# Kernel tuning notes

Hardware: AMD Instinct MI355X
Metric: run time of the kernel (lower is better)

The kernel has to match this reference:

```python
import jax, jax.numpy as jnp
import numpy as np

D_IN, D_OUT, H, L = 18, 2, 128, 2  # from load_pretrained config; bidirectional


def _uniform(key, shape, scale):
    return jax.random.uniform(key, shape, jnp.float32, -scale, scale)


def setup_inputs() -> dict:
    key = jax.random.key(0)
    ks = jax.random.split(key, 32)
    B, T = 64, 2048
    s = 1.0 / np.sqrt(H)
    inp = {"x": jax.random.normal(ks[0], (B, T, D_IN), jnp.float32)}
    i = 1
    for l in range(L):
        d_in_l = D_IN if l == 0 else 2 * H
        for suf in ("", "r"):
            inp[f"w_ih_l{l}{suf}"] = _uniform(ks[i], (3 * H, d_in_l), s); i += 1
            inp[f"w_hh_l{l}{suf}"] = _uniform(ks[i], (3 * H, H), s); i += 1
            inp[f"b_ih_l{l}{suf}"] = _uniform(ks[i], (3 * H,), s); i += 1
            inp[f"b_hh_l{l}{suf}"] = _uniform(ks[i], (3 * H,), s); i += 1
    inp["fc_w"] = _uniform(ks[i], (D_OUT, 2 * H), 1.0 / np.sqrt(2 * H)); i += 1
    inp["fc_b"] = _uniform(ks[i], (D_OUT,), 1.0 / np.sqrt(2 * H))
    return inp


def gru_dir(x, w_ih, w_hh, b_ih, b_hh, reverse):
    # x: [B,T,Din] -> [B,T,H], PyTorch GRU gate math (r,z,n ordering)
    B, T, _ = x.shape
    xg = jnp.einsum('btd,gd->btg', x, w_ih) + b_ih  # [B,T,3H], batched GEMM once
    if reverse:
        xg = xg[:, ::-1]
    def step(h, xt):
        gh = h @ w_hh.T + b_hh
        xr, xz, xn = jnp.split(xt, 3, axis=-1)
        hr, hz, hn = jnp.split(gh, 3, axis=-1)
        r = jax.nn.sigmoid(xr + hr)
        z = jax.nn.sigmoid(xz + hz)
        n = jnp.tanh(xn + r * hn)
        h_new = (1.0 - z) * n + z * h
        return h_new, h_new
    h0 = jnp.zeros((B, H), x.dtype)
    _, ys = jax.lax.scan(step, h0, jnp.swapaxes(xg, 0, 1))  # scan over time
    ys = jnp.swapaxes(ys, 0, 1)
    if reverse:
        ys = ys[:, ::-1]
    return ys


def gru_forward(x, params):
    h = x
    for l in range(L):
        fwd = gru_dir(h, params[f"w_ih_l{l}"], params[f"w_hh_l{l}"],
                      params[f"b_ih_l{l}"], params[f"b_hh_l{l}"], False)
        bwd = gru_dir(h, params[f"w_ih_l{l}r"], params[f"w_hh_l{l}r"],
                      params[f"b_ih_l{l}r"], params[f"b_hh_l{l}r"], True)
        h = jnp.concatenate([fwd, bwd], axis=-1)  # [B,T,2H]; dropout off (eval)
    return h


def reference(x, w_ih_l0, w_hh_l0, b_ih_l0, b_hh_l0,
              w_ih_l0r, w_hh_l0r, b_ih_l0r, b_hh_l0r,
              w_ih_l1, w_hh_l1, b_ih_l1, b_hh_l1,
              w_ih_l1r, w_hh_l1r, b_ih_l1r, b_hh_l1r,
              fc_w, fc_b):
    params = dict(w_ih_l0=w_ih_l0, w_hh_l0=w_hh_l0, b_ih_l0=b_ih_l0, b_hh_l0=b_hh_l0,
                  w_ih_l0r=w_ih_l0r, w_hh_l0r=w_hh_l0r, b_ih_l0r=b_ih_l0r, b_hh_l0r=b_hh_l0r,
                  w_ih_l1=w_ih_l1, w_hh_l1=w_hh_l1, b_ih_l1=b_ih_l1, b_hh_l1=b_hh_l1,
                  w_ih_l1r=w_ih_l1r, w_hh_l1r=w_hh_l1r, b_ih_l1r=b_ih_l1r, b_hh_l1r=b_hh_l1r)
    h = gru_forward(x, params)
    return jnp.einsum('bth,oh->bto', h, fc_w) + fc_b  # [B,T,D_OUT]
```

## Files before the change

### kernel.cpp

```cpp
#include <hip/hip_runtime.h>
#include <hip/hip_bf16.h>

#define B_   64
#define T_   2048
#define H_   128
#define G_   384
#define D0_  18
#define WIN  4
#define RING 8
#define NW   (T_ / WIN)

typedef __hip_bfloat16 bf16;
typedef __attribute__((ext_vector_type(4))) float f32x4;
typedef __attribute__((ext_vector_type(8))) short s16x8;

#define LOG2E  1.4426950408889634f
#define NEGL2E (-1.4426950408889634f)
#define TWOL2E (2.8853900817779268f)

__device__ __forceinline__ short f2bs(float v) {
    bf16 b = __float2bfloat16(v);
    return *reinterpret_cast<short*>(&b);
}
__device__ __forceinline__ unsigned short f2bu(float v) {
    bf16 b = __float2bfloat16(v);
    return *reinterpret_cast<unsigned short*>(&b);
}
__device__ __forceinline__ uint2 pk_bf16x4(float a, float b, float c, float d) {
    uint2 r;
    asm("v_cvt_pk_bf16_f32 %0, %1, %2" : "=v"(r.x) : "v"(a), "v"(b));
    asm("v_cvt_pk_bf16_f32 %0, %1, %2" : "=v"(r.y) : "v"(c), "v"(d));
    return r;
}
#define MFMA16(A, B, C) __builtin_amdgcn_mfma_f32_16x16x32_bf16((A), (B), (C), 0, 0, 0)

__device__ __forceinline__ void step_sync() {
    __asm__ volatile("s_waitcnt lgkmcnt(0)" ::: "memory");
    __builtin_amdgcn_s_barrier();
    __asm__ volatile("" ::: "memory");
}

__device__ __forceinline__ float gru_update(float yr, float yz, float aN,
                                            float aX, float h) {
    const float Er = __builtin_amdgcn_exp2f(yr);
    const float rg = __builtin_amdgcn_rcpf(1.0f + Er);
    const float En = __builtin_amdgcn_exp2f(fmaf(rg, aN, aX));
    const float Ez = __builtin_amdgcn_exp2f(yz);
    const float p  = fmaf(En, Ez, -Ez);
    const float q2 = fmaf(h, En, h);
    const float t1 = Ez + 1.0f;
    const float dn = fmaf(En, t1, t1);
    return (p + q2) * __builtin_amdgcn_rcpf(dn);
}


__global__ __launch_bounds__(512) void gru_l0_mfma(
    const float* __restrict__ x,
    const float* __restrict__ wih_f, const float* __restrict__ whh_f,
    const float* __restrict__ bih_f, const float* __restrict__ bhh_f,
    const float* __restrict__ wih_r, const float* __restrict__ whh_r,
    const float* __restrict__ bih_r, const float* __restrict__ bhh_r,
    bf16* __restrict__ l0h)
{
    __shared__ __align__(16) bf16 hring[RING][2048];
    __shared__ __align__(16) bf16 xbuf[2][WIN][512];

    const int bx   = blockIdx.x;
    const int dir  = bx >> 2;
    const int bg   = bx & 3;
    const int b0   = bg * 16;
    const int tid  = threadIdx.x;
    const int lane = tid & 63;
    const int wv   = tid >> 6;
    const int col  = lane & 15;
    const int quad = lane >> 4;

    const float* Wih = dir ? wih_r : wih_f;
    const float* Whh = dir ? whh_r : whh_f;
    const float* Bih = dir ? bih_r : bih_f;
    const float* Bhh = dir ? bhh_r : bhh_f;

    const float GSC[3] = {NEGL2E, NEGL2E, TWOL2E};

    s16x8 wfr[3][4], wxf[3];
    #pragma unroll
    for (int g = 0; g < 3; ++g) {
        const float sc = GSC[g];
        const float* wrow = Whh + (size_t)(g * H_ + wv * 16 + col) * H_;
        #pragma unroll
        for (int kt = 0; kt < 4; ++kt) {
            const float* p = wrow + kt * 32 + quad * 8;
            s16x8 f;
            #pragma unroll
            for (int i = 0; i < 8; ++i) f[i] = f2bs(p[i] * sc);
            wfr[g][kt] = f;
        }
        const float* xrow = Wih + (size_t)(g * H_ + wv * 16 + col) * D0_;
        s16x8 fx;
        #pragma unroll
        for (int i = 0; i < 8; ++i) {
            const int k = quad * 8 + i;
            fx[i] = (k < D0_) ? f2bs(xrow[k] * sc) : (short)0;
        }
        wxf[g] = fx;
    }
    f32x4 sR, sZ, sX, sN;
    #pragma unroll
    for (int r = 0; r < 4; ++r) {
        const int j = wv * 16 + quad * 4 + r;
        sR[r] = (Bih[j]        + Bhh[j])      * NEGL2E;
        sZ[r] = (Bih[H_ + j]   + Bhh[H_ + j]) * NEGL2E;
        sX[r] = Bih[2*H_ + j]  * TWOL2E;
        sN[r] = Bhh[2*H_ + j]  * TWOL2E;
    }

    const int wkt   = wv >> 1;
    const int wl    = (((wv << 1) + (quad >> 1)) & 3) * 16 + col;
    const int woff  = wkt * 512 + wl * 8 + (quad & 1) * 4;

    for (int i = tid; i < 2048; i += 512) hring[0][i] = __float2bfloat16(0.0f);
    #pragma unroll
    for (int k = 0; k < 4; ++k) {
        const int i = tid + k * 512;
        const int si = i >> 9, rem = i & 511;
        const int m = (rem >> 5) & 15, c = rem & 31;
        const int t = dir ? (T_ - 1 - si) : si;
        const float v = (c < D0_) ? x[((size_t)(b0 + m) * T_ + t) * D0_ + c] : 0.0f;
        xbuf[0][si][((c >> 3) * 16 + m) * 8 + (c & 7)] = __float2bfloat16(v);
    }
    __syncthreads();

    float hprev[4] = {0.f, 0.f, 0.f, 0.f};
    float xv[4];

    for (int w = 0; w < NW; ++w) {
        const int par = w & 1;
        s16x8 axf[WIN];
        #pragma unroll
        for (int si = 0; si < WIN; ++si)
            axf[si] = *(const s16x8*)&xbuf[par][si][lane * 8];

        #pragma unroll
        for (int si = 0; si < WIN; ++si) {
            const int s  = w * WIN + si;
            const int rb = s & (RING - 1);
            const int wb = (s + 1) & (RING - 1);

            s16x8 hfr[4];
            #pragma unroll
            for (int kt = 0; kt < 4; ++kt)
                hfr[kt] = *(const s16x8*)&hring[rb][kt * 512 + lane * 8];

            f32x4 aR = MFMA16(wxf[0], axf[si], sR);
            f32x4 aZ = MFMA16(wxf[1], axf[si], sZ);
            f32x4 aX = MFMA16(wxf[2], axf[si], sX);
            f32x4 aN = sN;
            #pragma unroll
            for (int kt = 0; kt < 4; ++kt) {
                aR = MFMA16(wfr[0][kt], hfr[kt], aR);
                aZ = MFMA16(wfr[1][kt], hfr[kt], aZ);
                aN = MFMA16(wfr[2][kt], hfr[kt], aN);
            }

            if (si == 1 && w > 0) {
                #pragma unroll
                for (int k = 0; k < 2; ++k) {
                    const int c  = tid + k * 512;
                    const int dt = c >> 8, m = (c >> 4) & 15, jo = c & 15;
                    const int fs = (w - 1) * WIN + dt;
                    const int t  = dir ? (T_ - 1 - fs) : fs;
                    const uint4 v = *(const uint4*)
                        &hring[(fs + 1) & (RING - 1)][(jo >> 2) * 512 + ((jo & 3) * 16 + m) * 8];
                    *(uint4*)(l0h + ((size_t)(b0 + m) * T_ + t) * 256 + dir * H_ + jo * 8) = v;
                }
            }

            if (si == 0 && w + 1 < NW) {
                #pragma unroll
                for (int k = 0; k < 4; ++k) {
                    const int i = tid + k * 512;
                    const int sj = i >> 9, rem = i & 511;
                    const int m = (rem >> 5) & 15, c = rem & 31;
                    const int s2 = (w + 1) * WIN + sj;
                    const int t2 = dir ? (T_ - 1 - s2) : s2;
                    xv[k] = (c < D0_) ? x[((size_t)(b0 + m) * T_ + t2) * D0_ + c] : 0.0f;
                }
            }

            float hn4[4];
            #pragma unroll
            for (int r = 0; r < 4; ++r) {
                const float hn = gru_update(aR[r], aZ[r], aN[r], aX[r], hprev[r]);
                hprev[r] = hn;
                hn4[r] = hn;
            }
            *(uint2*)&hring[wb][woff] = pk_bf16x4(hn4[0], hn4[1], hn4[2], hn4[3]);

            if (si == 3 && w + 1 < NW) {
                #pragma unroll
                for (int k = 0; k < 4; ++k) {
                    const int i = tid + k * 512;
                    const int sj = i >> 9, rem = i & 511;
                    const int m = (rem >> 5) & 15, c = rem & 31;
                    xbuf[par ^ 1][sj][((c >> 3) * 16 + m) * 8 + (c & 7)] =
                        __float2bfloat16(xv[k]);
                }
            }
            step_sync();
        }
    }
    #pragma unroll
    for (int k = 0; k < 2; ++k) {
        const int c  = tid + k * 512;
        const int dt = c >> 8, m = (c >> 4) & 15, jo = c & 15;
        const int fs = (NW - 1) * WIN + dt;
        const int t  = dir ? (T_ - 1 - fs) : fs;
        const uint4 v = *(const uint4*)
            &hring[(fs + 1) & (RING - 1)][(jo >> 2) * 512 + ((jo & 3) * 16 + m) * 8];
        *(uint4*)(l0h + ((size_t)(b0 + m) * T_ + t) * 256 + dir * H_ + jo * 8) = v;
    }
}

__global__ __launch_bounds__(256, 2) void xg_gemm_mfma(
    const bf16* __restrict__ A,
    const float* __restrict__ w_f, const float* __restrict__ w_r,
    const float* __restrict__ bi_f, const float* __restrict__ bi_r,
    const float* __restrict__ bh_f, const float* __restrict__ bh_r,
    bf16* __restrict__ xg_f, bf16* __restrict__ xg_r)
{
    __shared__ short As[128 * 40];
    __shared__ short Ws[128 * 40];
    __shared__ float Bias_s[128];

    const int dir  = blockIdx.z;
    const float* W   = dir ? w_r : w_f;
    const float* bi  = dir ? bi_r : bi_f;
    const float* bh  = dir ? bh_r : bh_f;
    bf16* xg         = dir ? xg_r : xg_f;

    const int tid  = threadIdx.x;
    const int lane = tid & 63;
    const int wv   = tid >> 6;
    const int col  = lane & 15;
    const int quad = lane >> 4;
    const int bx   = blockIdx.x;
    const int bg   = bx >> 8;
    const int t0   = (bx & 255) * 8;
    const int g    = blockIdx.y;
    const int m0   = g * 128;

    const float sc = (g < 2) ? NEGL2E : TWOL2E;
    const f32x4 z4 = {0.f, 0.f, 0.f, 0.f};

    if (tid < 128) {
        const int n = m0 + tid;
        Bias_s[tid] = (bi[n] + ((n < 2 * H_) ? bh[n] : 0.0f)) * sc;
    }

    f32x4 acc[2][8];
    #pragma unroll
    for (int mt = 0; mt < 2; ++mt)
        #pragma unroll
        for (int nt = 0; nt < 8; ++nt) acc[mt][nt] = z4;

    for (int k0 = 0; k0 < 256; k0 += 32) {
        #pragma unroll
        for (int i = 0; i < 2; ++i) {
            const int c = tid + i * 256;
            const int row = c >> 2, q4 = c & 3;
            const int dt = row >> 4, m = row & 15;
            *(uint4*)&As[row * 40 + q4 * 8] =
                *(const uint4*)(A + (((size_t)(bg * 16 + m) * T_ + t0 + dt) * 256)
                                + k0 + q4 * 8);
        }
        #pragma unroll
        for (int i = 0; i < 4; ++i) {
            const int c = tid + i * 256;
            const int row = c >> 3, q = c & 7;
            const float4 v = *(const float4*)(W + (size_t)(m0 + row) * 256 + k0 + q * 4);
            ushort4 u;
            u.x = f2bu(v.x * sc); u.y = f2bu(v.y * sc);
            u.z = f2bu(v.z * sc); u.w = f2bu(v.w * sc);
            *(ushort4*)&Ws[row * 40 + q * 4] = u;
        }
        __syncthreads();

        s16x8 wfr[2], hfr[8];
        #pragma unroll
        for (int mt = 0; mt < 2; ++mt)
            wfr[mt] = *(const s16x8*)&Ws[(wv * 32 + mt * 16 + col) * 40 + quad * 8];
        #pragma unroll
        for (int nt = 0; nt < 8; ++nt)
            hfr[nt] = *(const s16x8*)&As[(nt * 16 + col) * 40 + quad * 8];

        #pragma unroll
        for (int mt = 0; mt < 2; ++mt)
            #pragma unroll
            for (int nt = 0; nt < 8; ++nt)
                acc[mt][nt] = MFMA16(wfr[mt], hfr[nt], acc[mt][nt]);
        __syncthreads();
    }

    #pragma unroll
    for (int mt = 0; mt < 2; ++mt) {
        const int jt = wv * 2 + mt;
        float bv[4];
        #pragma unroll
        for (int r = 0; r < 4; ++r)
            bv[r] = Bias_s[wv * 32 + mt * 16 + quad * 4 + r];
        #pragma unroll
        for (int nt = 0; nt < 8; ++nt) {
            const uint2 o = pk_bf16x4(acc[mt][nt][0] + bv[0],
                                      acc[mt][nt][1] + bv[1],
                                      acc[mt][nt][2] + bv[2],
                                      acc[mt][nt][3] + bv[3]);
            const size_t idx = ((((size_t)bg * T_ + t0 + nt) * 3 + g) * 8 + jt) * 64
                             + quad * 16 + col;
            ((uint2*)xg)[idx] = o;
        }
    }
}

__global__ __launch_bounds__(512) void gru_l1_mfma(
    const bf16* __restrict__ xg_f, const bf16* __restrict__ xg_r,
    const float* __restrict__ whh_f, const float* __restrict__ bhh_f,
    const float* __restrict__ whh_r, const float* __restrict__ bhh_r,
    bf16* __restrict__ l1h, int fixed_dir)
{
    __shared__ __align__(16) bf16 hring[RING][2048];

    const int bx   = blockIdx.x;
    const int dir  = (fixed_dir >= 0) ? fixed_dir : (bx >> 2);
    const int bg   = bx & 3;
    const int b0   = bg * 16;
    const int tid  = threadIdx.x;
    const int lane = tid & 63;
    const int wv   = tid >> 6;
    const int col  = lane & 15;
    const int quad = lane >> 4;

    const bf16*  XG  = dir ? xg_r : xg_f;
    const float* Whh = dir ? whh_r : whh_f;
    const float* Bhh = dir ? bhh_r : bhh_f;

    const float GSC[3] = {NEGL2E, NEGL2E, TWOL2E};

    s16x8 wfr[3][4];
    #pragma unroll
    for (int g = 0; g < 3; ++g) {
        const float sc = GSC[g];
        const float* wrow = Whh + (size_t)(g * H_ + wv * 16 + col) * H_;
        #pragma unroll
        for (int kt = 0; kt < 4; ++kt) {
            const float* p = wrow + kt * 32 + quad * 8;
            s16x8 f;
            #pragma unroll
            for (int i = 0; i < 8; ++i) f[i] = f2bs(p[i] * sc);
            wfr[g][kt] = f;
        }
    }
    f32x4 sN;
    #pragma unroll
    for (int r = 0; r < 4; ++r)
        sN[r] = Bhh[2*H_ + wv * 16 + quad * 4 + r] * TWOL2E;

    const int wkt  = wv >> 1;
    const int wl   = (((wv << 1) + (quad >> 1)) & 3) * 16 + col;
    const int woff = wkt * 512 + wl * 8 + (quad & 1) * 4;

    for (int i = tid; i < 2048; i += 512) hring[0][i] = __float2bfloat16(0.0f);

    const uint2* xgb = (const uint2*)XG + ((size_t)bg * T_) * 3 * 8 * 64;
    const int lidx = wv * 64 + lane;

    uint2 xcur[WIN][3], xnxt[WIN][3];
    #pragma unroll
    for (int si = 0; si < WIN; ++si) {
        const int t = dir ? (T_ - 1 - si) : si;
        #pragma unroll
        for (int g = 0; g < 3; ++g)
            xcur[si][g] = xgb[((size_t)t * 3 + g) * 512 + lidx];
    }
    __syncthreads();

    float hprev[4] = {0.f, 0.f, 0.f, 0.f};

    for (int w = 0; w < NW; ++w) {
        #pragma unroll
        for (int si = 0; si < WIN; ++si) {
            const int s  = w * WIN + si;
            const int rb = s & (RING - 1);
            const int wb = (s + 1) & (RING - 1);

            s16x8 hfr[4];
            #pragma unroll
            for (int kt = 0; kt < 4; ++kt)
                hfr[kt] = *(const s16x8*)&hring[rb][kt * 512 + lane * 8];

            const uint2 xr2 = xcur[si][0], xz2 = xcur[si][1], xn2 = xcur[si][2];
            const f32x4 seedR = (f32x4){
                __uint_as_float(xr2.x << 16), __uint_as_float(xr2.x & 0xffff0000u),
                __uint_as_float(xr2.y << 16), __uint_as_float(xr2.y & 0xffff0000u)};
            const f32x4 seedZ = (f32x4){
                __uint_as_float(xz2.x << 16), __uint_as_float(xz2.x & 0xffff0000u),
                __uint_as_float(xz2.y << 16), __uint_as_float(xz2.y & 0xffff0000u)};
            const float xnf[4] = {
                __uint_as_float(xn2.x << 16), __uint_as_float(xn2.x & 0xffff0000u),
                __uint_as_float(xn2.y << 16), __uint_as_float(xn2.y & 0xffff0000u)};

            f32x4 aR = seedR, aZ = seedZ, aN = sN;
            #pragma unroll
            for (int kt = 0; kt < 4; ++kt) {
                aR = MFMA16(wfr[0][kt], hfr[kt], aR);
                aZ = MFMA16(wfr[1][kt], hfr[kt], aZ);
                aN = MFMA16(wfr[2][kt], hfr[kt], aN);
            }

            if (si == 1 && w > 0) {
                #pragma unroll
                for (int k = 0; k < 2; ++k) {
                    const int c  = tid + k * 512;
                    const int dt = c >> 8, m = (c >> 4) & 15, jo = c & 15;
                    const int fs = (w - 1) * WIN + dt;
                    const int t  = dir ? (T_ - 1 - fs) : fs;
                    const uint4 v = *(const uint4*)
                        &hring[(fs + 1) & (RING - 1)][(jo >> 2) * 512 + ((jo & 3) * 16 + m) * 8];
                    *(uint4*)(l1h + ((size_t)(b0 + m) * T_ + t) * 256 + dir * H_ + jo * 8) = v;
                }
            }

            if (si == 0 && w + 1 < NW) {
                #pragma unroll
                for (int sj = 0; sj < WIN; ++sj) {
                    const int s2 = (w + 1) * WIN + sj;
                    const int t2 = dir ? (T_ - 1 - s2) : s2;
                    #pragma unroll
                    for (int g = 0; g < 3; ++g)
                        xnxt[sj][g] = xgb[((size_t)t2 * 3 + g) * 512 + lidx];
                }
            }

            float hn4[4];
            #pragma unroll
            for (int r = 0; r < 4; ++r) {
                const float hn = gru_update(aR[r], aZ[r], aN[r], xnf[r], hprev[r]);
                hprev[r] = hn;
                hn4[r] = hn;
            }
            *(uint2*)&hring[wb][woff] = pk_bf16x4(hn4[0], hn4[1], hn4[2], hn4[3]);

            step_sync();
        }

        #pragma unroll
        for (int si = 0; si < WIN; ++si) {
            xcur[si][0] = xnxt[si][0];
            xcur[si][1] = xnxt[si][1];
            xcur[si][2] = xnxt[si][2];
        }
    }
    #pragma unroll
    for (int k = 0; k < 2; ++k) {
        const int c  = tid + k * 512;
        const int dt = c >> 8, m = (c >> 4) & 15, jo = c & 15;
        const int fs = (NW - 1) * WIN + dt;
        const int t  = dir ? (T_ - 1 - fs) : fs;
        const uint4 v = *(const uint4*)
            &hring[(fs + 1) & (RING - 1)][(jo >> 2) * 512 + ((jo & 3) * 16 + m) * 8];
        *(uint4*)(l1h + ((size_t)(b0 + m) * T_ + t) * 256 + dir * H_ + jo * 8) = v;
    }
}

__global__ __launch_bounds__(256, 2) void fc_kernel(
    const bf16* __restrict__ h, const float* __restrict__ fcw,
    const float* __restrict__ fcb, float* __restrict__ out)
{
    __shared__ float w0[256], w1[256];
    const int tid = threadIdx.x;
    w0[tid] = fcw[tid];
    w1[tid] = fcw[256 + tid];
    __syncthreads();

    const size_t bt = (size_t)blockIdx.x * 256 + tid;
    const bf16* hp = h + bt * 256;
    float s0 = fcb[0], s1 = fcb[1];
    #pragma unroll 4
    for (int k8 = 0; k8 < 32; ++k8) {
        const uint4 u = *(const uint4*)(hp + k8 * 8);
        const unsigned uu[4] = {u.x, u.y, u.z, u.w};
        #pragma unroll
        for (int p = 0; p < 4; ++p) {
            const float v0 = __uint_as_float(uu[p] << 16);
            const float v1 = __uint_as_float(uu[p] & 0xffff0000u);
            const int k = k8 * 8 + p * 2;
            s0 = fmaf(w0[k], v0, s0);     s1 = fmaf(w1[k], v0, s1);
            s0 = fmaf(w0[k + 1], v1, s0); s1 = fmaf(w1[k + 1], v1, s1);
        }
    }
    out[bt * 2]     = s0;
    out[bt * 2 + 1] = s1;
}

extern "C" void kernel_launch(void* const* d_in, const int* in_sizes, int n_in,
                              void* d_out, int out_size, void* d_ws, size_t ws_size,
                              hipStream_t stream)
{
    if (n_in < 19) return;
    const float* x     = (const float*)d_in[0];
    const float* wih0  = (const float*)d_in[1];
    const float* whh0  = (const float*)d_in[2];
    const float* bih0  = (const float*)d_in[3];
    const float* bhh0  = (const float*)d_in[4];
    const float* wih0r = (const float*)d_in[5];
    const float* whh0r = (const float*)d_in[6];
    const float* bih0r = (const float*)d_in[7];
    const float* bhh0r = (const float*)d_in[8];
    const float* wih1  = (const float*)d_in[9];
    const float* whh1  = (const float*)d_in[10];
    const float* bih1  = (const float*)d_in[11];
    const float* bhh1  = (const float*)d_in[12];
    const float* wih1r = (const float*)d_in[13];
    const float* whh1r = (const float*)d_in[14];
    const float* bih1r = (const float*)d_in[15];
    const float* bhh1r = (const float*)d_in[16];
    const float* fcw   = (const float*)d_in[17];
    const float* fcb   = (const float*)d_in[18];
    float* out = (float*)d_out;

    const size_t nBT  = (size_t)B_ * T_;
    const size_t hh_b = nBT * 2 * H_ * sizeof(bf16);
    const size_t xg_b = nBT * G_ * sizeof(bf16);
    const size_t xg_el = nBT * G_;

    if (ws_size >= hh_b + 2 * xg_b) {
        bf16* l0h = (bf16*)d_ws;
        bf16* xgf = (bf16*)((char*)d_ws + hh_b);
        bf16* xgr = xgf + xg_el;

        gru_l0_mfma<<<dim3(8), dim3(512), 0, stream>>>(
            x, wih0, whh0, bih0, bhh0, wih0r, whh0r, bih0r, bhh0r, l0h);
        xg_gemm_mfma<<<dim3(1024, 3, 2), dim3(256), 0, stream>>>(
            l0h, wih1, wih1r, bih1, bih1r, bhh1, bhh1r, xgf, xgr);
        gru_l1_mfma<<<dim3(8), dim3(512), 0, stream>>>(
            xgf, xgr, whh1, bhh1, whh1r, bhh1r, l0h, -1);
        fc_kernel<<<dim3((int)(nBT / 256)), dim3(256), 0, stream>>>(l0h, fcw, fcb, out);
    } else if (ws_size >= 2 * hh_b + xg_b) {
        bf16* l0h = (bf16*)d_ws;
        bf16* xg  = (bf16*)((char*)d_ws + hh_b);
        bf16* l1h = (bf16*)((char*)d_ws + hh_b + xg_b);

        gru_l0_mfma<<<dim3(8), dim3(512), 0, stream>>>(
            x, wih0, whh0, bih0, bhh0, wih0r, whh0r, bih0r, bhh0r, l0h);
        xg_gemm_mfma<<<dim3(1024, 3, 1), dim3(256), 0, stream>>>(
            l0h, wih1, wih1, bih1, bih1, bhh1, bhh1, xg, xg);
        gru_l1_mfma<<<dim3(4), dim3(512), 0, stream>>>(
            xg, xg, whh1, bhh1, whh1r, bhh1r, l1h, 0);
        xg_gemm_mfma<<<dim3(1024, 3, 1), dim3(256), 0, stream>>>(
            l0h, wih1r, wih1r, bih1r, bih1r, bhh1r, bhh1r, xg, xg);
        gru_l1_mfma<<<dim3(4), dim3(512), 0, stream>>>(
            xg, xg, whh1, bhh1, whh1r, bhh1r, l1h, 1);
        fc_kernel<<<dim3((int)(nBT / 256)), dim3(256), 0, stream>>>(l1h, fcw, fcb, out);
    }
}
```

Baseline: 2.509 ms.

## Duplicate recurrent MFMA across two wave halves to split gate updates

Both recurrent GRU kernels now run 1024 threads per block instead of 512. The upper eight waves redundantly compute the same MFMA tiles as the lower eight, and each half applies the gate nonlinearity to only two of the four accumulator rows, writing packed bf16 pairs. The aim is to halve the serial transcendental and update work on the per-step critical path and to spread the output and prefetch stores over more threads. The cost is doubled MFMA issue, more register pressure under the 1024-thread bound, and a wider barrier every step.

```diff
diff --git a/kernel.cpp b/kernel.cpp
--- a/kernel.cpp
+++ b/kernel.cpp
@@ -25,6 +25,11 @@
 __device__ __forceinline__ unsigned short f2bu(float v) {
     bf16 b = __float2bfloat16(v);
     return *reinterpret_cast<unsigned short*>(&b);
+}
+__device__ __forceinline__ unsigned pk_bf16x2(float a, float b) {
+    unsigned r;
+    asm("v_cvt_pk_bf16_f32 %0, %1, %2" : "=v"(r) : "v"(a), "v"(b));
+    return r;
 }
 __device__ __forceinline__ uint2 pk_bf16x4(float a, float b, float c, float d) {
     uint2 r;
@@ -54,7 +59,7 @@
 }
 
 
-__global__ __launch_bounds__(512) void gru_l0_mfma(
+__global__ __launch_bounds__(1024) void gru_l0_mfma(
     const float* __restrict__ x,
     const float* __restrict__ wih_f, const float* __restrict__ whh_f,
     const float* __restrict__ bih_f, const float* __restrict__ bhh_f,
@@ -71,7 +76,8 @@
     const int b0   = bg * 16;
     const int tid  = threadIdx.x;
     const int lane = tid & 63;
-    const int wv   = tid >> 6;
+    const int wv   = (tid >> 6) & 7;
+    const int half = tid >> 9;
     const int col  = lane & 15;
     const int quad = lane >> 4;
 
@@ -116,12 +122,12 @@
 
     const int wkt   = wv >> 1;
     const int wl    = (((wv << 1) + (quad >> 1)) & 3) * 16 + col;
-    const int woff  = wkt * 512 + wl * 8 + (quad & 1) * 4;
-
-    for (int i = tid; i < 2048; i += 512) hring[0][i] = __float2bfloat16(0.0f);
-    #pragma unroll
-    for (int k = 0; k < 4; ++k) {
-        const int i = tid + k * 512;
+    const int woff  = wkt * 512 + wl * 8 + (quad & 1) * 4 + half * 2;
+
+    for (int i = tid; i < 2048; i += 1024) hring[0][i] = __float2bfloat16(0.0f);
+    #pragma unroll
+    for (int k = 0; k < 2; ++k) {
+        const int i = tid + k * 1024;
         const int si = i >> 9, rem = i & 511;
         const int m = (rem >> 5) & 15, c = rem & 31;
         const int t = dir ? (T_ - 1 - si) : si;
@@ -130,8 +136,8 @@
     }
     __syncthreads();
 
-    float hprev[4] = {0.f, 0.f, 0.f, 0.f};
-    float xv[4];
+    float hprev[2] = {0.f, 0.f};
+    float xv[2];
 
     for (int w = 0; w < NW; ++w) {
         const int par = w & 1;
@@ -163,22 +169,19 @@
             }
 
             if (si == 1 && w > 0) {
+                const int c  = tid;
+                const int dt = c >> 8, m = (c >> 4) & 15, jo = c & 15;
+                const int fs = (w - 1) * WIN + dt;
+                const int t  = dir ? (T_ - 1 - fs) : fs;
+                const uint4 v = *(const uint4*)
+                    &hring[(fs + 1) & (RING - 1)][(jo >> 2) * 512 + ((jo & 3) * 16 + m) * 8];
+                *(uint4*)(l0h + ((size_t)(b0 + m) * T_ + t) * 256 + dir * H_ + jo * 8) = v;
+            }
+
+            if (si == 0 && w + 1 < NW) {
                 #pragma unroll
                 for (int k = 0; k < 2; ++k) {
-                    const int c  = tid + k * 512;
-                    const int dt = c >> 8, m = (c >> 4) & 15, jo = c & 15;
-                    const int fs = (w - 1) * WIN + dt;
-                    const int t  = dir ? (T_ - 1 - fs) : fs;
-                    const uint4 v = *(const uint4*)
-                        &hring[(fs + 1) & (RING - 1)][(jo >> 2) * 512 + ((jo & 3) * 16 + m) * 8];
-                    *(uint4*)(l0h + ((size_t)(b0 + m) * T_ + t) * 256 + dir * H_ + jo * 8) = v;
-                }
-            }
-
-            if (si == 0 && w + 1 < NW) {
-                #pragma unroll
-                for (int k = 0; k < 4; ++k) {
-                    const int i = tid + k * 512;
+                    const int i = tid + k * 1024;
                     const int sj = i >> 9, rem = i & 511;
                     const int m = (rem >> 5) & 15, c = rem & 31;
                     const int s2 = (w + 1) * WIN + sj;
@@ -187,19 +190,19 @@
                 }
             }
 
-            float hn4[4];
-            #pragma unroll
-            for (int r = 0; r < 4; ++r) {
-                const float hn = gru_update(aR[r], aZ[r], aN[r], aX[r], hprev[r]);
-                hprev[r] = hn;
-                hn4[r] = hn;
-            }
-            *(uint2*)&hring[wb][woff] = pk_bf16x4(hn4[0], hn4[1], hn4[2], hn4[3]);
+            const float yr0 = half ? aR[2] : aR[0], yr1 = half ? aR[3] : aR[1];
+            const float yz0 = half ? aZ[2] : aZ[0], yz1 = half ? aZ[3] : aZ[1];
+            const float an0 = half ? aN[2] : aN[0], an1 = half ? aN[3] : aN[1];
+            const float ax0 = half ? aX[2] : aX[0], ax1 = half ? aX[3] : aX[1];
+            const float hn0 = gru_update(yr0, yz0, an0, ax0, hprev[0]);
+            const float hn1 = gru_update(yr1, yz1, an1, ax1, hprev[1]);
+            hprev[0] = hn0; hprev[1] = hn1;
+            *(unsigned*)&hring[wb][woff] = pk_bf16x2(hn0, hn1);
 
             if (si == 3 && w + 1 < NW) {
                 #pragma unroll
-                for (int k = 0; k < 4; ++k) {
-                    const int i = tid + k * 512;
+                for (int k = 0; k < 2; ++k) {
+                    const int i = tid + k * 1024;
                     const int sj = i >> 9, rem = i & 511;
                     const int m = (rem >> 5) & 15, c = rem & 31;
                     xbuf[par ^ 1][sj][((c >> 3) * 16 + m) * 8 + (c & 7)] =
@@ -209,9 +212,8 @@
             step_sync();
         }
     }
-    #pragma unroll
-    for (int k = 0; k < 2; ++k) {
-        const int c  = tid + k * 512;
+    {
+        const int c  = tid;
         const int dt = c >> 8, m = (c >> 4) & 15, jo = c & 15;
         const int fs = (NW - 1) * WIN + dt;
         const int t  = dir ? (T_ - 1 - fs) : fs;
@@ -321,7 +323,7 @@
     }
 }
 
-__global__ __launch_bounds__(512) void gru_l1_mfma(
+__global__ __launch_bounds__(1024) void gru_l1_mfma(
     const bf16* __restrict__ xg_f, const bf16* __restrict__ xg_r,
     const float* __restrict__ whh_f, const float* __restrict__ bhh_f,
     const float* __restrict__ whh_r, const float* __restrict__ bhh_r,
@@ -335,7 +337,8 @@
     const int b0   = bg * 16;
     const int tid  = threadIdx.x;
     const int lane = tid & 63;
-    const int wv   = tid >> 6;
+    const int wv   = (tid >> 6) & 7;
+    const int half = tid >> 9;
     const int col  = lane & 15;
     const int quad = lane >> 4;
 
@@ -366,9 +369,9 @@
 
     const int wkt  = wv >> 1;
     const int wl   = (((wv << 1) + (quad >> 1)) & 3) * 16 + col;
-    const int woff = wkt * 512 + wl * 8 + (quad & 1) * 4;
-
-    for (int i = tid; i < 2048; i += 512) hring[0][i] = __float2bfloat16(0.0f);
+    const int woff = wkt * 512 + wl * 8 + (quad & 1) * 4 + half * 2;
+
+    for (int i = tid; i < 2048; i += 1024) hring[0][i] = __float2bfloat16(0.0f);
 
     const uint2* xgb = (const uint2*)XG + ((size_t)bg * T_) * 3 * 8 * 64;
     const int lidx = wv * 64 + lane;
@@ -383,7 +386,7 @@
     }
     __syncthreads();
 
-    float hprev[4] = {0.f, 0.f, 0.f, 0.f};
+    float hprev[2] = {0.f, 0.f};
 
     for (int w = 0; w < NW; ++w) {
         #pragma unroll
@@ -404,7 +407,7 @@
             const f32x4 seedZ = (f32x4){
                 __uint_as_float(xz2.x << 16), __uint_as_float(xz2.x & 0xffff0000u),
                 __uint_as_float(xz2.y << 16), __uint_as_float(xz2.y & 0xffff0000u)};
-            const float xnf[4] = {
+            const f32x4 xnf = (f32x4){
                 __uint_as_float(xn2.x << 16), __uint_as_float(xn2.x & 0xffff0000u),
                 __uint_as_float(xn2.y << 16), __uint_as_float(xn2.y & 0xffff0000u)};
 
@@ -417,16 +420,13 @@
             }
 
             if (si == 1 && w > 0) {
-                #pragma unroll
-                for (int k = 0; k < 2; ++k) {
-                    const int c  = tid + k * 512;
-                    const int dt = c >> 8, m = (c >> 4) & 15, jo = c & 15;
-                    const int fs = (w - 1) * WIN + dt;
-                    const int t  = dir ? (T_ - 1 - fs) : fs;
-                    const uint4 v = *(const uint4*)
-                        &hring[(fs + 1) & (RING - 1)][(jo >> 2) * 512 + ((jo & 3) * 16 + m) * 8];
-                    *(uint4*)(l1h + ((size_t)(b0 + m) * T_ + t) * 256 + dir * H_ + jo * 8) = v;
-                }
+                const int c  = tid;
+                const int dt = c >> 8, m = (c >> 4) & 15, jo = c & 15;
+                const int fs = (w - 1) * WIN + dt;
+                const int t  = dir ? (T_ - 1 - fs) : fs;
+                const uint4 v = *(const uint4*)
+                    &hring[(fs + 1) & (RING - 1)][(jo >> 2) * 512 + ((jo & 3) * 16 + m) * 8];
+                *(uint4*)(l1h + ((size_t)(b0 + m) * T_ + t) * 256 + dir * H_ + jo * 8) = v;
             }
 
             if (si == 0 && w + 1 < NW) {
@@ -440,14 +440,14 @@
                 }
             }
 
-            float hn4[4];
-            #pragma unroll
-            for (int r = 0; r < 4; ++r) {
-                const float hn = gru_update(aR[r], aZ[r], aN[r], xnf[r], hprev[r]);
-                hprev[r] = hn;
-                hn4[r] = hn;
-            }
-            *(uint2*)&hring[wb][woff] = pk_bf16x4(hn4[0], hn4[1], hn4[2], hn4[3]);
+            const float yr0 = half ? aR[2] : aR[0], yr1 = half ? aR[3] : aR[1];
+            const float yz0 = half ? aZ[2] : aZ[0], yz1 = half ? aZ[3] : aZ[1];
+            const float an0 = half ? aN[2] : aN[0], an1 = half ? aN[3] : aN[1];
+            const float ax0 = half ? xnf[2] : xnf[0], ax1 = half ? xnf[3] : xnf[1];
+            const float hn0 = gru_update(yr0, yz0, an0, ax0, hprev[0]);
+            const float hn1 = gru_update(yr1, yz1, an1, ax1, hprev[1]);
+            hprev[0] = hn0; hprev[1] = hn1;
+            *(unsigned*)&hring[wb][woff] = pk_bf16x2(hn0, hn1);
 
             step_sync();
         }
@@ -459,9 +459,8 @@
             xcur[si][2] = xnxt[si][2];
         }
     }
-    #pragma unroll
-    for (int k = 0; k < 2; ++k) {
-        const int c  = tid + k * 512;
+    {
+        const int c  = tid;
         const int dt = c >> 8, m = (c >> 4) & 15, jo = c & 15;
         const int fs = (NW - 1) * WIN + dt;
         const int t  = dir ? (T_ - 1 - fs) : fs;
@@ -537,11 +536,11 @@
         bf16* xgf = (bf16*)((char*)d_ws + hh_b);
         bf16* xgr = xgf + xg_el;
 
-        gru_l0_mfma<<<dim3(8), dim3(512), 0, stream>>>(
+        gru_l0_mfma<<<dim3(8), dim3(1024), 0, stream>>>(
             x, wih0, whh0, bih0, bhh0, wih0r, whh0r, bih0r, bhh0r, l0h);
         xg_gemm_mfma<<<dim3(1024, 3, 2), dim3(256), 0, stream>>>(
             l0h, wih1, wih1r, bih1, bih1r, bhh1, bhh1r, xgf, xgr);
-        gru_l1_mfma<<<dim3(8), dim3(512), 0, stream>>>(
+        gru_l1_mfma<<<dim3(8), dim3(1024), 0, stream>>>(
             xgf, xgr, whh1, bhh1, whh1r, bhh1r, l0h, -1);
         fc_kernel<<<dim3((int)(nBT / 256)), dim3(256), 0, stream>>>(l0h, fcw, fcb, out);
     } else if (ws_size >= 2 * hh_b + xg_b) {
@@ -549,15 +548,15 @@
         bf16* xg  = (bf16*)((char*)d_ws + hh_b);
         bf16* l1h = (bf16*)((char*)d_ws + hh_b + xg_b);
 
-        gru_l0_mfma<<<dim3(8), dim3(512), 0, stream>>>(
+        gru_l0_mfma<<<dim3(8), dim3(1024), 0, stream>>>(
             x, wih0, whh0, bih0, bhh0, wih0r, whh0r, bih0r, bhh0r, l0h);
         xg_gemm_mfma<<<dim3(1024, 3, 1), dim3(256), 0, stream>>>(
             l0h, wih1, wih1, bih1, bih1, bhh1, bhh1, xg, xg);
-        gru_l1_mfma<<<dim3(4), dim3(512), 0, stream>>>(
+        gru_l1_mfma<<<dim3(4), dim3(1024), 0, stream>>>(
             xg, xg, whh1, bhh1, whh1r, bhh1r, l1h, 0);
         xg_gemm_mfma<<<dim3(1024, 3, 1), dim3(256), 0, stream>>>(
             l0h, wih1r, wih1r, bih1r, bih1r, bhh1r, bhh1r, xg, xg);
-        gru_l1_mfma<<<dim3(4), dim3(512), 0, stream>>>(
+        gru_l1_mfma<<<dim3(4), dim3(1024), 0, stream>>>(
             xg, xg, whh1, bhh1, whh1r, bhh1r, l1h, 1);
         fc_kernel<<<dim3((int)(nBT / 256)), dim3(256), 0, stream>>>(l1h, fcw, fcb, out);
     }
```

After: 3.961 ms. 1.58x slower.
